# Kernel tuning notes

Hardware: AMD Instinct MI355X
Metric: run time of the kernel (lower is better)

## Reference

```python
import jax, jax.numpy as jnp
import numpy as np

T_TOKENS = 4096      # batch*seq_len
HIDDEN = 2048
N_EXPERTS = 8
TOP_K = 2


def setup_inputs() -> dict:
    key = jax.random.key(0)
    k1, k2 = jax.random.split(key)
    hidden_states = jax.random.normal(k1, (T_TOKENS, HIDDEN), dtype=jnp.float32)
    # nn.Linear(hidden_size, num_experts) weight: [E, H]
    w_router = jax.random.normal(k2, (N_EXPERTS, HIDDEN), dtype=jnp.float32) * (1.0 / np.sqrt(HIDDEN))
    return {"hidden_states": hidden_states, "w_router": w_router, "top_k": TOP_K}


def reference(hidden_states, w_router, top_k):
    T, H = hidden_states.shape
    E = w_router.shape[0]
    # router_logits = linear_router(hidden_states.float())  -> [T, E]
    logits = jnp.einsum("th,eh->te", hidden_states.astype(jnp.float32), w_router)
    # topk along expert dim (torch does this in fp64; ordering/values identical for fp32 inputs)
    top_val, top_idx = jax.lax.top_k(logits, top_k)  # [T, k], [T, k]
    # scatter top values into a dense [T, E] grid of -inf, then transpose -> [E, T]
    rows = jnp.arange(T)[:, None]
    scores_te = jnp.full((T, E), -jnp.inf, dtype=jnp.float32).at[rows, top_idx].set(top_val)
    router_scores = jax.nn.sigmoid(scores_te).T  # [E, T]; sigmoid(-inf) == 0
    # router_indices: arange(T) broadcast to [E, T], flattened, expanded across hidden dim
    router_indices = jnp.broadcast_to(jnp.arange(T, dtype=jnp.int32)[None, :], (E, T))
    router_indices = jnp.broadcast_to(router_indices.reshape(-1, 1), (E * T, H))  # [E*T, H]
    router_probs = router_scores.reshape(-1, 1)  # [E*T, 1]
    return (router_scores, router_indices, router_probs)
```

## Files before the change

### kernel.cpp

```cpp
#include <hip/hip_runtime.h>
#include <math.h>

#define T_TOKENS 4096
#define HIDDEN   2048
#define N_EXPERTS 8

__global__ __launch_bounds__(256) void fill_indices_kernel(float* __restrict__ out1)
{
    const int n4 = (N_EXPERTS * T_TOKENS * HIDDEN) / 4;
    float4* o4 = (float4*)out1;
    int stride = gridDim.x * blockDim.x;
    for (int i = blockIdx.x * blockDim.x + threadIdx.x; i < n4; i += stride) {
        float v = (float)((i >> 9) & (T_TOKENS - 1));
        o4[i] = make_float4(v, v, v, v);
    }
}

__global__ __launch_bounds__(256) void router_scores_kernel(
    const float* __restrict__ h, const float* __restrict__ w,
    float* __restrict__ out0, float* __restrict__ out2)
{
    __shared__ float wlds[N_EXPERTS * HIDDEN];
    const float4* w4  = (const float4*)w;
    float4*       wl4 = (float4*)wlds;
    for (int i = threadIdx.x; i < (N_EXPERTS * HIDDEN) / 4; i += 256)
        wl4[i] = w4[i];
    __syncthreads();

    const int wave = threadIdx.x >> 6;
    const int lane = threadIdx.x & 63;
    const int t = blockIdx.x * 4 + wave;

    const float4* h4 = (const float4*)(h + (size_t)t * HIDDEN);
    float acc[N_EXPERTS];
    #pragma unroll
    for (int e = 0; e < N_EXPERTS; e++) acc[e] = 0.f;

    #pragma unroll
    for (int k = 0; k < 8; k++) {
        float4 hv = h4[k * 64 + lane];
        #pragma unroll
        for (int e = 0; e < N_EXPERTS; e++) {
            float4 wv = wl4[e * 512 + k * 64 + lane];
            acc[e] += hv.x * wv.x + hv.y * wv.y + hv.z * wv.z + hv.w * wv.w;
        }
    }

    #pragma unroll
    for (int e = 0; e < N_EXPERTS; e++) {
        #pragma unroll
        for (int off = 32; off > 0; off >>= 1)
            acc[e] += __shfl_down(acc[e], off, 64);
    }

    if (lane == 0) {
        int i1 = 0; float v1 = acc[0];
        #pragma unroll
        for (int e = 1; e < N_EXPERTS; e++)
            if (acc[e] > v1) { v1 = acc[e]; i1 = e; }
        int i2 = -1; float v2 = -INFINITY;
        #pragma unroll
        for (int e = 0; e < N_EXPERTS; e++)
            if (e != i1 && acc[e] > v2) { v2 = acc[e]; i2 = e; }

        float s1 = 1.f / (1.f + expf(-v1));
        float s2 = 1.f / (1.f + expf(-v2));

        #pragma unroll
        for (int e = 0; e < N_EXPERTS; e++) {
            float val = (e == i1) ? s1 : ((e == i2) ? s2 : 0.f);
            out0[e * T_TOKENS + t] = val;
            out2[e * T_TOKENS + t] = val;
        }
    }
}

extern "C" void kernel_launch(void* const* d_in, const int* in_sizes, int n_in,
                              void* d_out, int out_size, void* d_ws, size_t ws_size,
                              hipStream_t stream) {
    const float* h = (const float*)d_in[0];
    const float* w = (const float*)d_in[1];

    float* out  = (float*)d_out;
    float* out0 = out;
    float* out1 = out + N_EXPERTS * T_TOKENS;
    float* out2 = out1 + (size_t)N_EXPERTS * T_TOKENS * HIDDEN;

    hipLaunchKernelGGL(fill_indices_kernel, dim3(8192), dim3(256), 0, stream, out1);
    hipLaunchKernelGGL(router_scores_kernel, dim3(1024), dim3(256), 0, stream,
                       h, w, out0, out2);
}
```

Baseline: 296.3 us.

## Fuse router score computation and index fill into one interleaved kernel

Merges the index-fill kernel and the router-score kernel into a single launch. Every eighth block computes scores for 16 tokens, four per wave, reading the weights directly from global memory instead of staging them in LDS. The other blocks fill the broadcast index tensor, one row per wave. This removes a launch, lets the small matmul overlap the large write-bound fill, and reuses each weight load across four tokens. The cost is more registers per compute wave and uncoalesced weight reads that depend on the cache.

```diff
diff --git a/kernel.cpp b/kernel.cpp
--- a/kernel.cpp
+++ b/kernel.cpp
@@ -4,73 +4,94 @@
 #define T_TOKENS 4096
 #define HIDDEN   2048
 #define N_EXPERTS 8
+#define N_ROWS   (N_EXPERTS * T_TOKENS)
+#define ROW_F4   (HIDDEN / 4)
 
-__global__ __launch_bounds__(256) void fill_indices_kernel(float* __restrict__ out1)
+#define NBLOCKS     2048
+#define FILL_BLOCKS 1792
+#define FILL_WAVES  (FILL_BLOCKS * 4)
+
+__global__ __launch_bounds__(256) void fused_router_fill(
+    const float* __restrict__ h, const float* __restrict__ w,
+    float* __restrict__ out0, float* __restrict__ out1, float* __restrict__ out2)
 {
-    const int n4 = (N_EXPERTS * T_TOKENS * HIDDEN) / 4;
-    float4* o4 = (float4*)out1;
-    int stride = gridDim.x * blockDim.x;
-    for (int i = blockIdx.x * blockDim.x + threadIdx.x; i < n4; i += stride) {
-        float v = (float)((i >> 9) & (T_TOKENS - 1));
-        o4[i] = make_float4(v, v, v, v);
-    }
-}
-
-__global__ __launch_bounds__(256) void router_scores_kernel(
-    const float* __restrict__ h, const float* __restrict__ w,
-    float* __restrict__ out0, float* __restrict__ out2)
-{
-    __shared__ float wlds[N_EXPERTS * HIDDEN];
-    const float4* w4  = (const float4*)w;
-    float4*       wl4 = (float4*)wlds;
-    for (int i = threadIdx.x; i < (N_EXPERTS * HIDDEN) / 4; i += 256)
-        wl4[i] = w4[i];
-    __syncthreads();
-
+    const int bid  = blockIdx.x;
     const int wave = threadIdx.x >> 6;
     const int lane = threadIdx.x & 63;
-    const int t = blockIdx.x * 4 + wave;
 
-    const float4* h4 = (const float4*)(h + (size_t)t * HIDDEN);
-    float acc[N_EXPERTS];
-    #pragma unroll
-    for (int e = 0; e < N_EXPERTS; e++) acc[e] = 0.f;
+    if ((bid & 7) == 0) {
+        const int rb = bid >> 3;
+        const int t0 = rb * 16 + wave * 4;
 
-    #pragma unroll
-    for (int k = 0; k < 8; k++) {
-        float4 hv = h4[k * 64 + lane];
+        const float4* h4 = (const float4*)h;
+        const float4* w4 = (const float4*)w;
+
+        float acc[4][N_EXPERTS];
         #pragma unroll
-        for (int e = 0; e < N_EXPERTS; e++) {
-            float4 wv = wl4[e * 512 + k * 64 + lane];
-            acc[e] += hv.x * wv.x + hv.y * wv.y + hv.z * wv.z + hv.w * wv.w;
-        }
-    }
-
-    #pragma unroll
-    for (int e = 0; e < N_EXPERTS; e++) {
-        #pragma unroll
-        for (int off = 32; off > 0; off >>= 1)
-            acc[e] += __shfl_down(acc[e], off, 64);
-    }
-
-    if (lane == 0) {
-        int i1 = 0; float v1 = acc[0];
-        #pragma unroll
-        for (int e = 1; e < N_EXPERTS; e++)
-            if (acc[e] > v1) { v1 = acc[e]; i1 = e; }
-        int i2 = -1; float v2 = -INFINITY;
-        #pragma unroll
-        for (int e = 0; e < N_EXPERTS; e++)
-            if (e != i1 && acc[e] > v2) { v2 = acc[e]; i2 = e; }
-
-        float s1 = 1.f / (1.f + expf(-v1));
-        float s2 = 1.f / (1.f + expf(-v2));
+        for (int t = 0; t < 4; t++)
+            #pragma unroll
+            for (int e = 0; e < N_EXPERTS; e++) acc[t][e] = 0.f;
 
         #pragma unroll
-        for (int e = 0; e < N_EXPERTS; e++) {
-            float val = (e == i1) ? s1 : ((e == i2) ? s2 : 0.f);
-            out0[e * T_TOKENS + t] = val;
-            out2[e * T_TOKENS + t] = val;
+        for (int k = 0; k < 8; k++) {
+            float4 hv[4];
+            #pragma unroll
+            for (int t = 0; t < 4; t++)
+                hv[t] = h4[(size_t)(t0 + t) * ROW_F4 + k * 64 + lane];
+            #pragma unroll
+            for (int e = 0; e < N_EXPERTS; e++) {
+                float4 wv = w4[e * ROW_F4 + k * 64 + lane];
+                #pragma unroll
+                for (int t = 0; t < 4; t++)
+                    acc[t][e] += hv[t].x * wv.x + hv[t].y * wv.y
+                               + hv[t].z * wv.z + hv[t].w * wv.w;
+            }
+        }
+
+        #pragma unroll
+        for (int t = 0; t < 4; t++)
+            #pragma unroll
+            for (int e = 0; e < N_EXPERTS; e++)
+                #pragma unroll
+                for (int off = 32; off > 0; off >>= 1)
+                    acc[t][e] += __shfl_down(acc[t][e], off, 64);
+
+        if (lane == 0) {
+            #pragma unroll
+            for (int t = 0; t < 4; t++) {
+                const int tok = t0 + t;
+                int i1 = 0; float v1 = acc[t][0];
+                #pragma unroll
+                for (int e = 1; e < N_EXPERTS; e++)
+                    if (acc[t][e] > v1) { v1 = acc[t][e]; i1 = e; }
+                int i2 = -1; float v2 = -INFINITY;
+                #pragma unroll
+                for (int e = 0; e < N_EXPERTS; e++)
+                    if (e != i1 && acc[t][e] > v2) { v2 = acc[t][e]; i2 = e; }
+
+                float s1 = 1.f / (1.f + expf(-v1));
+                float s2 = 1.f / (1.f + expf(-v2));
+
+                #pragma unroll
+                for (int e = 0; e < N_EXPERTS; e++) {
+                    float val = (e == i1) ? s1 : ((e == i2) ? s2 : 0.f);
+                    out0[e * T_TOKENS + tok] = val;
+                    out2[e * T_TOKENS + tok] = val;
+                }
+            }
+        }
+    } else {
+        const int fb    = (bid >> 3) * 7 + (bid & 7) - 1;
+        const int fwave = fb * 4 + wave;
+        float4* o4 = (float4*)out1;
+
+        for (int r = fwave; r < N_ROWS; r += FILL_WAVES) {
+            float v = (float)(r & (T_TOKENS - 1));
+            float4 vv = make_float4(v, v, v, v);
+            float4* rowp = o4 + (size_t)r * ROW_F4;
+            #pragma unroll
+            for (int j = 0; j < 8; j++)
+                rowp[j * 64 + lane] = vv;
         }
     }
 }
@@ -86,7 +107,6 @@
     float* out1 = out + N_EXPERTS * T_TOKENS;
     float* out2 = out1 + (size_t)N_EXPERTS * T_TOKENS * HIDDEN;
 
-    hipLaunchKernelGGL(fill_indices_kernel, dim3(8192), dim3(256), 0, stream, out1);
-    hipLaunchKernelGGL(router_scores_kernel, dim3(1024), dim3(256), 0, stream,
-                       h, w, out0, out2);
+    hipLaunchKernelGGL(fused_router_fill, dim3(NBLOCKS), dim3(256), 0, stream,
+                       h, w, out0, out1, out2);
 }
```

Result: slower. 365.3 us (+23.3%).

## Fuse index fill and router scoring into one kernel with interleaved writes

Applied to the files above, without the earlier changes.

Merges the large index-fill kernel and the router-score kernel into a single launch. Each wave fills four rows of the index output, and the first 4096 waves also load a token's hidden row before the fill and compute its logits afterwards. The router work then overlaps with the write-bandwidth-bound fill, and one kernel launch is removed. The weights are now read straight from global memory (L2-cached) instead of being staged in LDS, and only the first half of the blocks do router work, so load may be uneven across blocks.

```diff
diff --git a/kernel.cpp b/kernel.cpp
--- a/kernel.cpp
+++ b/kernel.cpp
@@ -4,73 +4,85 @@
 #define T_TOKENS 4096
 #define HIDDEN   2048
 #define N_EXPERTS 8
+#define N_ROWS   (N_EXPERTS * T_TOKENS)
+#define ROW_F4   (HIDDEN / 4)
 
-__global__ __launch_bounds__(256) void fill_indices_kernel(float* __restrict__ out1)
+#define NBLOCKS 2048
+
+__global__ __launch_bounds__(256) void fused_router_fill(
+    const float* __restrict__ h, const float* __restrict__ w,
+    float* __restrict__ out0, float* __restrict__ out1, float* __restrict__ out2)
 {
-    const int n4 = (N_EXPERTS * T_TOKENS * HIDDEN) / 4;
-    float4* o4 = (float4*)out1;
-    int stride = gridDim.x * blockDim.x;
-    for (int i = blockIdx.x * blockDim.x + threadIdx.x; i < n4; i += stride) {
-        float v = (float)((i >> 9) & (T_TOKENS - 1));
-        o4[i] = make_float4(v, v, v, v);
-    }
-}
-
-__global__ __launch_bounds__(256) void router_scores_kernel(
-    const float* __restrict__ h, const float* __restrict__ w,
-    float* __restrict__ out0, float* __restrict__ out2)
-{
-    __shared__ float wlds[N_EXPERTS * HIDDEN];
-    const float4* w4  = (const float4*)w;
-    float4*       wl4 = (float4*)wlds;
-    for (int i = threadIdx.x; i < (N_EXPERTS * HIDDEN) / 4; i += 256)
-        wl4[i] = w4[i];
-    __syncthreads();
-
     const int wave = threadIdx.x >> 6;
     const int lane = threadIdx.x & 63;
-    const int t = blockIdx.x * 4 + wave;
+    const int gw   = blockIdx.x * 4 + wave;
+    const bool is_router = (gw < T_TOKENS);
 
-    const float4* h4 = (const float4*)(h + (size_t)t * HIDDEN);
-    float acc[N_EXPERTS];
-    #pragma unroll
-    for (int e = 0; e < N_EXPERTS; e++) acc[e] = 0.f;
+    const float4* h4 = (const float4*)h;
+    const float4* w4 = (const float4*)w;
 
-    #pragma unroll
-    for (int k = 0; k < 8; k++) {
-        float4 hv = h4[k * 64 + lane];
+    float4 hv[8];
+    if (is_router) {
         #pragma unroll
-        for (int e = 0; e < N_EXPERTS; e++) {
-            float4 wv = wl4[e * 512 + k * 64 + lane];
-            acc[e] += hv.x * wv.x + hv.y * wv.y + hv.z * wv.z + hv.w * wv.w;
+        for (int j = 0; j < 8; j++)
+            hv[j] = h4[(size_t)gw * ROW_F4 + j * 64 + lane];
+    }
+
+    {
+        float4* o4 = (float4*)out1;
+        const int r0 = gw * 4;
+        #pragma unroll
+        for (int i = 0; i < 4; i++) {
+            float v = (float)((r0 + i) & (T_TOKENS - 1));
+            float4 vv = make_float4(v, v, v, v);
+            float4* rowp = o4 + (size_t)(r0 + i) * ROW_F4;
+            #pragma unroll
+            for (int j = 0; j < 8; j++)
+                rowp[j * 64 + lane] = vv;
         }
     }
 
-    #pragma unroll
-    for (int e = 0; e < N_EXPERTS; e++) {
+    if (is_router) {
+        float acc[N_EXPERTS];
         #pragma unroll
-        for (int off = 32; off > 0; off >>= 1)
-            acc[e] += __shfl_down(acc[e], off, 64);
-    }
-
-    if (lane == 0) {
-        int i1 = 0; float v1 = acc[0];
-        #pragma unroll
-        for (int e = 1; e < N_EXPERTS; e++)
-            if (acc[e] > v1) { v1 = acc[e]; i1 = e; }
-        int i2 = -1; float v2 = -INFINITY;
-        #pragma unroll
-        for (int e = 0; e < N_EXPERTS; e++)
-            if (e != i1 && acc[e] > v2) { v2 = acc[e]; i2 = e; }
-
-        float s1 = 1.f / (1.f + expf(-v1));
-        float s2 = 1.f / (1.f + expf(-v2));
+        for (int e = 0; e < N_EXPERTS; e++) acc[e] = 0.f;
 
         #pragma unroll
         for (int e = 0; e < N_EXPERTS; e++) {
-            float val = (e == i1) ? s1 : ((e == i2) ? s2 : 0.f);
-            out0[e * T_TOKENS + t] = val;
-            out2[e * T_TOKENS + t] = val;
+            #pragma unroll
+            for (int j = 0; j < 8; j++) {
+                float4 wv = w4[e * ROW_F4 + j * 64 + lane];
+                acc[e] += hv[j].x * wv.x + hv[j].y * wv.y
+                        + hv[j].z * wv.z + hv[j].w * wv.w;
+            }
+        }
+
+        #pragma unroll
+        for (int e = 0; e < N_EXPERTS; e++) {
+            #pragma unroll
+            for (int off = 32; off > 0; off >>= 1)
+                acc[e] += __shfl_down(acc[e], off, 64);
+        }
+
+        if (lane == 0) {
+            int i1 = 0; float v1 = acc[0];
+            #pragma unroll
+            for (int e = 1; e < N_EXPERTS; e++)
+                if (acc[e] > v1) { v1 = acc[e]; i1 = e; }
+            int i2 = -1; float v2 = -INFINITY;
+            #pragma unroll
+            for (int e = 0; e < N_EXPERTS; e++)
+                if (e != i1 && acc[e] > v2) { v2 = acc[e]; i2 = e; }
+
+            float s1 = 1.f / (1.f + expf(-v1));
+            float s2 = 1.f / (1.f + expf(-v2));
+
+            #pragma unroll
+            for (int e = 0; e < N_EXPERTS; e++) {
+                float val = (e == i1) ? s1 : ((e == i2) ? s2 : 0.f);
+                out0[e * T_TOKENS + gw] = val;
+                out2[e * T_TOKENS + gw] = val;
+            }
         }
     }
 }
@@ -86,7 +98,6 @@
     float* out1 = out + N_EXPERTS * T_TOKENS;
     float* out2 = out1 + (size_t)N_EXPERTS * T_TOKENS * HIDDEN;
 
-    hipLaunchKernelGGL(fill_indices_kernel, dim3(8192), dim3(256), 0, stream, out1);
-    hipLaunchKernelGGL(router_scores_kernel, dim3(1024), dim3(256), 0, stream,
-                       h, w, out0, out2);
+    hipLaunchKernelGGL(fused_router_fill, dim3(NBLOCKS), dim3(256), 0, stream,
+                       h, w, out0, out1, out2);
 }
```

New measurement: 302.2 us. Within noise of the previous version (+2.0%).
